# Optimization experiments

Measured on AMD Instinct MI355X. Metric: run time of the kernel, lower is better.

## Reference

```python
import jax, jax.numpy as jnp
import numpy as np

D_MODEL = 2048
N_HEAD = 16
N_KV_HEAD = 4
D_HEAD = D_MODEL // N_HEAD  # 128
WINDOW = 512
B, T = 2, 2048


def _rope_tables(T, d_head, base=10000.0):
    inv = 1.0 / (base ** (np.arange(0, d_head, 2, dtype=np.float32) / d_head))
    t = np.arange(T, dtype=np.float32)
    freqs = np.outer(t, inv)  # [T, d_head//2]
    return jnp.asarray(np.cos(freqs)), jnp.asarray(np.sin(freqs))


def setup_inputs() -> dict:
    key = jax.random.key(0)
    ks = jax.random.split(key, 5)
    cos, sin = _rope_tables(T, D_HEAD)
    s = 1.0 / np.sqrt(D_MODEL)
    return {
        "x": jax.random.normal(ks[0], (B, T, D_MODEL), jnp.float32),
        "cos": cos,
        "sin": sin,
        "Wq": jax.random.normal(ks[1], (D_MODEL, D_MODEL), jnp.float32) * s,
        "Wk": jax.random.normal(ks[2], (D_MODEL, N_KV_HEAD * D_HEAD), jnp.float32) * s,
        "Wv": jax.random.normal(ks[3], (D_MODEL, N_KV_HEAD * D_HEAD), jnp.float32) * s,
        "Wo": jax.random.normal(ks[4], (D_MODEL, D_MODEL), jnp.float32) * s,
    }


def _apply_rope(t, cos, sin):
    # t: [B, T, H, D]; cos/sin: [T, D//2]; interleaved-pair (complex) rotation
    tr = t[..., 0::2]
    ti = t[..., 1::2]
    c = cos[None, :, None, :]
    s = sin[None, :, None, :]
    out_r = tr * c - ti * s
    out_i = tr * s + ti * c
    return jnp.stack([out_r, out_i], axis=-1).reshape(t.shape)


def reference(x, cos, sin, Wq, Wk, Wv, Wo):
    Bx, Tx, C = x.shape
    q = (x @ Wq).reshape(Bx, Tx, N_HEAD, D_HEAD)       # [B,T,H,D]
    k = (x @ Wk).reshape(Bx, Tx, N_KV_HEAD, D_HEAD)    # [B,T,Hkv,D]
    v = (x @ Wv).reshape(Bx, Tx, N_KV_HEAD, D_HEAD)
    q = _apply_rope(q, cos, sin)
    k = _apply_rope(k, cos, sin)
    n_rep = N_HEAD // N_KV_HEAD
    k = jnp.repeat(k, n_rep, axis=2)  # [B,T,H,D]
    v = jnp.repeat(v, n_rep, axis=2)
    scale = 1.0 / np.sqrt(D_HEAD)
    att = jnp.einsum("bihd,bjhd->bhij", q, k) * scale  # [B,H,T,T]
    i = jnp.arange(Tx)[:, None]
    j = jnp.arange(Tx)[None, :]
    mask = (j <= i) & (j >= i - WINDOW + 1)            # causal sliding window
    att = jnp.where(mask[None, None], att, -jnp.inf)
    att = jax.nn.softmax(att, axis=-1)
    y = jnp.einsum("bhij,bjhd->bihd", att, v).reshape(Bx, Tx, C)
    return y @ Wo
```

## Files before the change

kernel.cpp:

```cpp
#include <hip/hip_runtime.h>
#include <hip/hip_bf16.h>
#include <cstdint>
#include <cstddef>

#define B_ 2
#define T_ 2048
#define NH 16
#define NKV 4
#define DH 128
#define DM 2048
#define WIN 512

typedef __attribute__((ext_vector_type(4))) float f32x4;
typedef __attribute__((ext_vector_type(8))) __bf16 bf16x8;

using bf16 = __hip_bfloat16;

__device__ inline void gload_lds16(const void* g, void* l) {
  __builtin_amdgcn_global_load_lds(
      (const __attribute__((address_space(1))) void*)g,
      (__attribute__((address_space(3))) void*)l, 16, 0, 0);
}

__device__ inline unsigned pack_bf2(float a, float b) {
  unsigned short ua = __builtin_bit_cast(unsigned short, __float2bfloat16(a));
  unsigned short ub = __builtin_bit_cast(unsigned short, __float2bfloat16(b));
  return (unsigned)ua | ((unsigned)ub << 16);
}

#define FBAR()                           \
  do {                                   \
    asm volatile("" ::: "memory");       \
    __builtin_amdgcn_s_barrier();        \
    asm volatile("" ::: "memory");       \
  } while (0)

__global__ void k_f32_to_bf16(const float* __restrict__ in, bf16* __restrict__ out, int n) {
  int i = (blockIdx.x * blockDim.x + threadIdx.x) * 4;
  if (i >= n) return;
  float4 v = *(const float4*)(in + i);
  ushort4 o;
  o.x = __builtin_bit_cast(unsigned short, __float2bfloat16(v.x));
  o.y = __builtin_bit_cast(unsigned short, __float2bfloat16(v.y));
  o.z = __builtin_bit_cast(unsigned short, __float2bfloat16(v.z));
  o.w = __builtin_bit_cast(unsigned short, __float2bfloat16(v.w));
  *(ushort4*)(out + i) = o;
}

__global__ __launch_bounds__(256) void k_transpose_bf16(const float* __restrict__ W,
                                                        bf16* __restrict__ Wt, int K, int N) {
  __shared__ float tile[64][65];
  int n0 = blockIdx.x * 64, k0 = blockIdx.y * 64;
  int tx = threadIdx.x & 63, tg = threadIdx.x >> 6;
#pragma unroll
  for (int r = 0; r < 16; ++r) {
    int k = tg * 16 + r;
    tile[k][tx] = W[(size_t)(k0 + k) * N + n0 + tx];
  }
  __syncthreads();
#pragma unroll
  for (int r = 0; r < 16; ++r) {
    int nn = tg * 16 + r;
    Wt[(size_t)(n0 + nn) * K + k0 + tx] = __float2bfloat16(tile[tx][nn]);
  }
}

template <int BN, bool OUT_BF16>
__global__ __launch_bounds__(512, 2) void k_gemm8(const bf16* __restrict__ A,
                                                  const bf16* __restrict__ Bt,
                                                  void* __restrict__ Cout,
                                                  int M, int N, int K) {
  constexpr int NR = BN / 64;
  constexpr int NHF = NR / 2;
  constexpr int BISS = BN / 128;
  __shared__ __align__(16) char As_[2][32768];
  __shared__ __align__(16) char Bs_[2][BN * 128];

  const int tid = threadIdx.x;
  const int w = tid >> 6, lane = tid & 63;
  const int li = lane & 15, g = lane >> 4;
  const int wm = w >> 2, wn = w & 3;

  const int nwg = gridDim.x * gridDim.y;
  int bid = blockIdx.y * gridDim.x + blockIdx.x;
  bid = (bid & 7) * (nwg >> 3) + (bid >> 3);
  const int m0 = (bid / gridDim.x) * 256;
  const int n0 = (bid % gridDim.x) * BN;

  const int ntiles = K >> 6;
  const int NT2 = ntiles >> 1;

  auto sA = [&](int buf, int tile, int half, int issue) {
    if (tile >= ntiles) return;
    const int R0 = half * 64 + issue * 128;
    const int rr = R0 + w * 8 + (lane >> 3);
    const int sl = lane & 7;
    const bf16* src = A + (size_t)(m0 + rr) * K + tile * 64 + ((sl ^ (rr & 7)) * 8);
    gload_lds16(src, As_[buf] + (R0 + w * 8) * 128);
  };
  auto sB = [&](int buf, int tile, int half, int issue) {
    if (tile >= ntiles) return;
    const int bb = issue * 8 + w;
    const int block = (BN == 256) ? ((bb >> 2) * 8 + (bb & 3) + half * 4)
                                  : ((bb >> 1) * 4 + (bb & 1) + half * 2);
    const int rr = block * 8 + (lane >> 3);
    const int sl = lane & 7;
    const bf16* src = Bt + (size_t)(n0 + rr) * K + tile * 64 + ((sl ^ (rr & 7)) * 8);
    gload_lds16(src, Bs_[buf] + block * 1024);
  };

  const int swz0 = (g ^ (li & 7)) * 16;
  const int swz1 = ((4 + g) ^ (li & 7)) * 16;
  bf16x8 af[8], b0v[NHF * 2], b1v[NHF * 2];
  f32x4 acc[8][NR] = {};

  auto readA = [&](int buf, int mh) {
#pragma unroll
    for (int m = 0; m < 4; ++m) {
      const char* p = As_[buf] + (wm * 128 + mh * 64 + m * 16 + li) * 128;
      af[m * 2 + 0] = *(const bf16x8*)(p + swz0);
      af[m * 2 + 1] = *(const bf16x8*)(p + swz1);
    }
  };
  auto readB = [&](int buf, int nh, bf16x8* bv) {
#pragma unroll
    for (int n = 0; n < NHF; ++n) {
      const char* p = Bs_[buf] + (wn * (NR * 16) + nh * (NHF * 16) + n * 16 + li) * 128;
      bv[n * 2 + 0] = *(const bf16x8*)(p + swz0);
      bv[n * 2 + 1] = *(const bf16x8*)(p + swz1);
    }
  };
  auto MMA = [&](int mh, int nh, const bf16x8* bv) {
    __builtin_amdgcn_s_setprio(1);
#pragma unroll
    for (int m = 0; m < 4; ++m)
#pragma unroll
      for (int n = 0; n < NHF; ++n)
#pragma unroll
        for (int kk = 0; kk < 2; ++kk)
          acc[mh * 4 + m][nh * NHF + n] = __builtin_amdgcn_mfma_f32_16x16x32_bf16(
              af[m * 2 + kk], bv[n * 2 + kk], acc[mh * 4 + m][nh * NHF + n], 0, 0, 0);
    __builtin_amdgcn_s_setprio(0);
  };
  auto VMW = [&](bool last) {
    if (last) {
      asm volatile("s_waitcnt vmcnt(0)" ::: "memory");
    } else {
      if constexpr (BN == 256)
        asm volatile("s_waitcnt vmcnt(4)" ::: "memory");
      else
        asm volatile("s_waitcnt vmcnt(3)" ::: "memory");
    }
    __builtin_amdgcn_sched_barrier(0);
  };

  sA(0, 0, 0, 0); sA(0, 0, 0, 1); sA(0, 0, 1, 0); sA(0, 0, 1, 1);
  sB(0, 0, 0, 0); if constexpr (BISS == 2) sB(0, 0, 0, 1);
  sB(0, 0, 1, 0); if constexpr (BISS == 2) sB(0, 0, 1, 1);
  sA(1, 1, 0, 0); sA(1, 1, 0, 1);
  sB(1, 1, 0, 0); if constexpr (BISS == 2) sB(1, 1, 0, 1);
  if constexpr (BN == 256)
    asm volatile("s_waitcnt vmcnt(4)" ::: "memory");
  else
    asm volatile("s_waitcnt vmcnt(3)" ::: "memory");
  __builtin_amdgcn_sched_barrier(0);
  FBAR();

  for (int itr = 0; itr < NT2; ++itr) {
    const int t = itr * 2;
    const bool last = (itr == NT2 - 1);
    readA(0, 0); readB(0, 0, b0v);
    sA(1, t + 1, 1, 0); sA(1, t + 1, 1, 1);
    FBAR(); MMA(0, 0, b0v); FBAR();
    readB(0, 1, b1v);
    sB(1, t + 1, 1, 0); if constexpr (BISS == 2) sB(1, t + 1, 1, 1);
    FBAR(); MMA(0, 1, b1v); FBAR();
    readA(0, 1);
    sA(0, t + 2, 0, 0); sA(0, t + 2, 0, 1);
    FBAR(); MMA(1, 0, b0v); FBAR();
    sB(0, t + 2, 0, 0); if constexpr (BISS == 2) sB(0, t + 2, 0, 1);
    VMW(last);
    FBAR(); MMA(1, 1, b1v); FBAR();
    readA(1, 0); readB(1, 0, b0v);
    sA(0, t + 2, 1, 0); sA(0, t + 2, 1, 1);
    FBAR(); MMA(0, 0, b0v); FBAR();
    readB(1, 1, b1v);
    sB(0, t + 2, 1, 0); if constexpr (BISS == 2) sB(0, t + 2, 1, 1);
    FBAR(); MMA(0, 1, b1v); FBAR();
    readA(1, 1);
    sA(1, t + 3, 0, 0); sA(1, t + 3, 0, 1);
    FBAR(); MMA(1, 0, b0v); FBAR();
    sB(1, t + 3, 0, 0); if constexpr (BISS == 2) sB(1, t + 3, 0, 1);
    VMW(last);
    FBAR(); MMA(1, 1, b1v); FBAR();
  }

#pragma unroll
  for (int mf = 0; mf < 8; ++mf)
#pragma unroll
    for (int nf = 0; nf < NR; ++nf)
#pragma unroll
      for (int r = 0; r < 4; ++r) {
        int row = m0 + wm * 128 + mf * 16 + g * 4 + r;
        int col = n0 + wn * (NR * 16) + nf * 16 + li;
        float v = acc[mf][nf][r];
        if constexpr (OUT_BF16)
          ((bf16*)Cout)[(size_t)row * N + col] = __float2bfloat16(v);
        else
          ((float*)Cout)[(size_t)row * N + col] = v;
      }
}

__global__ void k_rope_qkv(bf16* __restrict__ qkv, const float* __restrict__ cosT,
                           const float* __restrict__ sinT) {
  int p = blockIdx.x * blockDim.x + threadIdx.x;
  int i = p & 63;
  int h20 = (p >> 6) % 20;
  int bt = p / (64 * 20);
  int t = bt & (T_ - 1);
  float c = cosT[t * 64 + i], s = sinT[t * 64 + i];
  bool isq = h20 < 16;
  int col = isq ? h20 * DH : DM + (h20 - 16) * DH;
  float sc = isq ? 0.08838834764831845f : 1.0f;
  size_t base = (size_t)bt * 3072 + col + 2 * i;
  float tr = __bfloat162float(qkv[base]);
  float ti = __bfloat162float(qkv[base + 1]);
  qkv[base] = __float2bfloat16((tr * c - ti * s) * sc);
  qkv[base + 1] = __float2bfloat16((tr * s + ti * c) * sc);
}

__global__ __launch_bounds__(256) void k_vtrans(const bf16* __restrict__ qkv,
                                                bf16* __restrict__ vt) {
  __shared__ bf16 tile[64][72];
  int bt0 = blockIdx.x * 64, c0 = blockIdx.y * 64;
  int tx = threadIdx.x & 63, tg = threadIdx.x >> 6;
#pragma unroll
  for (int r = 0; r < 16; ++r) {
    int row = tg * 16 + r;
    tile[row][tx] = qkv[(size_t)(bt0 + row) * 3072 + 2560 + c0 + tx];
  }
  __syncthreads();
#pragma unroll
  for (int r = 0; r < 16; ++r) {
    int row2 = tg * 16 + r;
    vt[(size_t)(c0 + row2) * (B_ * T_) + bt0 + tx] = tile[tx][row2];
  }
}

__global__ __launch_bounds__(512) void k_attn(const bf16* __restrict__ qkv,
                                              const bf16* __restrict__ vt,
                                              bf16* __restrict__ Y) {
  __shared__ __align__(16) char Ks[2][9216];
  __shared__ __align__(16) char Vs[2][10240];
  __shared__ __align__(16) char Pl[8][1280];
  const int lane = threadIdx.x & 63;
  const int w = threadIdx.x >> 6;
  const int li = lane & 15, g = lane >> 4;
  const int t0 = ((int)gridDim.x - 1 - (int)blockIdx.x) * 32;
  const int b = blockIdx.y / NKV, kvh = blockIdx.y % NKV;
  const int h = kvh * 4 + (w >> 1);
  const int qrow0 = t0 + (w & 1) * 16;
  const int t = qrow0 + li;

  bf16x8 qf[4];
  const bf16* qbase = qkv + (size_t)(b * T_ + qrow0 + li) * 3072 + h * DH;
#pragma unroll
  for (int dk = 0; dk < 4; ++dk) qf[dk] = *(const bf16x8*)(qbase + dk * 32 + g * 8);

  float mrow = -1e4f;
  float srow = 0.f;
  f32x4 acc[8] = {};

  int ks0 = t0 - (WIN - 1);
  if (ks0 < 0) ks0 = 0;
  ks0 &= ~31;
  const int nt = (t0 + 31 - ks0) / 32 + 1;

  const bf16* kgbase = qkv + (size_t)(b * T_) * 3072 + DM + kvh * DH;
  const bf16* vgbase = vt + (size_t)(kvh * DH) * (B_ * T_) + b * T_;

  auto STAGE = [&](int buf, int kt) {
    for (int c = w; c < 19; c += 8) {
      if (c < 9) {
        int slot = c * 64 + lane;
        int row = slot / 17, cc = slot % 17;
        if (slot >= 544) { row = 0; cc = 0; }
        if (cc == 16) cc = 0;
        const bf16* src = kgbase + (size_t)(kt + row) * 3072 + cc * 8;
        gload_lds16(src, Ks[buf] + c * 1024);
      } else {
        int c2 = c - 9;
        int slot = c2 * 64 + lane;
        int row = slot / 5, cc = slot % 5;
        if (cc == 4) cc = 0;
        const bf16* src = vgbase + (size_t)row * (B_ * T_) + kt + cc * 8;
        gload_lds16(src, Vs[buf] + c2 * 1024);
      }
    }
  };

  STAGE(0, ks0);
  __syncthreads();
  int cur = 0;

  for (int it = 0; it < nt; ++it) {
    const int kt = ks0 + it * 32;
    if (it + 1 < nt) STAGE(cur ^ 1, kt + 32);

    f32x4 sc[2] = {};
#pragma unroll
    for (int n = 0; n < 2; ++n)
#pragma unroll
      for (int dk = 0; dk < 4; ++dk) {
        bf16x8 kf = *(const bf16x8*)(Ks[cur] + (n * 16 + li) * 272 + dk * 64 + g * 16);
        sc[n] = __builtin_amdgcn_mfma_f32_16x16x32_bf16(kf, qf[dk], sc[n], 0, 0, 0);
      }

    float p[2][4];
    float pmax = -1e30f;
#pragma unroll
    for (int n = 0; n < 2; ++n)
#pragma unroll
      for (int r = 0; r < 4; ++r) {
        int key = kt + n * 16 + g * 4 + r;
        bool valid = (key <= t) && (key > t - WIN);
        float pv = valid ? sc[n][r] : -1e30f;
        p[n][r] = pv;
        pmax = fmaxf(pmax, pv);
      }
    pmax = fmaxf(pmax, __shfl_xor(pmax, 16));
    pmax = fmaxf(pmax, __shfl_xor(pmax, 32));

    float nm = fmaxf(mrow, pmax);
    float alpha = __expf(mrow - nm);
    mrow = nm;
    float rs = 0.f;
#pragma unroll
    for (int n = 0; n < 2; ++n)
#pragma unroll
      for (int r = 0; r < 4; ++r) {
        p[n][r] = __expf(p[n][r] - nm);
        rs += p[n][r];
      }
    rs += __shfl_xor(rs, 16);
    rs += __shfl_xor(rs, 32);
    srow = srow * alpha + rs;

#pragma unroll
    for (int n = 0; n < 2; ++n) {
      *(unsigned*)(Pl[w] + li * 80 + n * 32 + g * 8) = pack_bf2(p[n][0], p[n][1]);
      *(unsigned*)(Pl[w] + li * 80 + n * 32 + g * 8 + 4) = pack_bf2(p[n][2], p[n][3]);
    }

    float af_[4];
#pragma unroll
    for (int r = 0; r < 4; ++r) af_[r] = __shfl(alpha, (g << 2) + r);
#pragma unroll
    for (int db = 0; db < 8; ++db)
#pragma unroll
      for (int r = 0; r < 4; ++r) acc[db][r] *= af_[r];

    bf16x8 pf = *(const bf16x8*)(Pl[w] + li * 80 + g * 16);
#pragma unroll
    for (int db = 0; db < 8; ++db) {
      bf16x8 vf = *(const bf16x8*)(Vs[cur] + (db * 16 + li) * 80 + g * 16);
      acc[db] = __builtin_amdgcn_mfma_f32_16x16x32_bf16(pf, vf, acc[db], 0, 0, 0);
    }

    __syncthreads();
    cur ^= 1;
  }

  float inv[4];
#pragma unroll
  for (int r = 0; r < 4; ++r) inv[r] = 1.f / __shfl(srow, (g << 2) + r);
  bf16* ybase = Y + (size_t)(b * T_ + qrow0 + (g << 2)) * DM + h * DH;
#pragma unroll
  for (int r = 0; r < 4; ++r)
#pragma unroll
    for (int db = 0; db < 8; ++db)
      ybase[(size_t)r * DM + db * 16 + li] = __float2bfloat16(acc[db][r] * inv[r]);
}

extern "C" void kernel_launch(void* const* d_in, const int* in_sizes, int n_in,
                              void* d_out, int out_size, void* d_ws, size_t ws_size,
                              hipStream_t stream) {
  const float* x = (const float*)d_in[0];
  const float* cosT = (const float*)d_in[1];
  const float* sinT = (const float*)d_in[2];
  const float* Wq = (const float*)d_in[3];
  const float* Wk = (const float*)d_in[4];
  const float* Wv = (const float*)d_in[5];
  const float* Wo = (const float*)d_in[6];
  float* out = (float*)d_out;

  char* ws = (char*)d_ws;
  bf16* xb = (bf16*)ws;     ws += (size_t)4096 * 2048 * 2;
  bf16* Wqkvt = (bf16*)ws;  ws += (size_t)3072 * 2048 * 2;
  bf16* Wot = (bf16*)ws;    ws += (size_t)2048 * 2048 * 2;
  bf16* qkv = (bf16*)ws;    ws += (size_t)4096 * 3072 * 2;
  bf16* yb = xb;
  bf16* vt = Wqkvt;

  k_f32_to_bf16<<<(4096 * 2048 / 4 + 255) / 256, 256, 0, stream>>>(x, xb, 4096 * 2048);
  k_transpose_bf16<<<dim3(2048 / 64, 2048 / 64), 256, 0, stream>>>(Wq, Wqkvt, 2048, 2048);
  k_transpose_bf16<<<dim3(512 / 64, 2048 / 64), 256, 0, stream>>>(Wk, Wqkvt + (size_t)2048 * 2048, 2048, 512);
  k_transpose_bf16<<<dim3(512 / 64, 2048 / 64), 256, 0, stream>>>(Wv, Wqkvt + (size_t)2560 * 2048, 2048, 512);
  k_transpose_bf16<<<dim3(2048 / 64, 2048 / 64), 256, 0, stream>>>(Wo, Wot, 2048, 2048);

  k_gemm8<256, true><<<dim3(3072 / 256, 4096 / 256), 512, 0, stream>>>(xb, Wqkvt, qkv, 4096, 3072, 2048);

  k_rope_qkv<<<(4096 * 20 * 64) / 256, 256, 0, stream>>>(qkv, cosT, sinT);
  k_vtrans<<<dim3(4096 / 64, 512 / 64), 256, 0, stream>>>(qkv, vt);

  k_attn<<<dim3(T_ / 32, B_ * NKV), 512, 0, stream>>>(qkv, vt, yb);

  k_gemm8<128, false><<<dim3(2048 / 128, 4096 / 256), 512, 0, stream>>>(yb, Wot, out, 4096, 2048, 2048);
}
```

Before: 183.6 us.

## Fuse prep and rope/vtrans launches and use 192-wide QKV GEMM tile

Merges the x conversion and four weight transposes into one kernel, and rope with the V transpose into another, cutting launch overhead. Generalizes the GEMM B-tile loader to support an uneven split, so the QKV GEMM can use a 192-wide tile giving 256 workgroups to better fill the GPU. Risk: uneven wave work and a different vmcnt accounting in the pipeline.

```diff
diff --git a/kernel.cpp b/kernel.cpp
--- a/kernel.cpp
+++ b/kernel.cpp
@@ -35,23 +35,41 @@
     asm volatile("" ::: "memory");       \
   } while (0)
 
-__global__ void k_f32_to_bf16(const float* __restrict__ in, bf16* __restrict__ out, int n) {
-  int i = (blockIdx.x * blockDim.x + threadIdx.x) * 4;
-  if (i >= n) return;
-  float4 v = *(const float4*)(in + i);
-  ushort4 o;
-  o.x = __builtin_bit_cast(unsigned short, __float2bfloat16(v.x));
-  o.y = __builtin_bit_cast(unsigned short, __float2bfloat16(v.y));
-  o.z = __builtin_bit_cast(unsigned short, __float2bfloat16(v.z));
-  o.w = __builtin_bit_cast(unsigned short, __float2bfloat16(v.w));
-  *(ushort4*)(out + i) = o;
-}
-
-__global__ __launch_bounds__(256) void k_transpose_bf16(const float* __restrict__ W,
-                                                        bf16* __restrict__ Wt, int K, int N) {
+__global__ __launch_bounds__(256) void k_prep(const float* __restrict__ x,
+                                              const float* __restrict__ Wq,
+                                              const float* __restrict__ Wk,
+                                              const float* __restrict__ Wv,
+                                              const float* __restrict__ Wo,
+                                              bf16* __restrict__ xb,
+                                              bf16* __restrict__ Wqkvt,
+                                              bf16* __restrict__ Wot) {
+  int id = blockIdx.x;
+  int tid = threadIdx.x;
+  if (id >= 2560) {
+    size_t base = (size_t)(id - 2560) * 4096 + tid * 16;
+#pragma unroll
+    for (int j = 0; j < 4; ++j) {
+      float4 v = *(const float4*)(x + base + j * 4);
+      ushort4 o;
+      o.x = __builtin_bit_cast(unsigned short, __float2bfloat16(v.x));
+      o.y = __builtin_bit_cast(unsigned short, __float2bfloat16(v.y));
+      o.z = __builtin_bit_cast(unsigned short, __float2bfloat16(v.z));
+      o.w = __builtin_bit_cast(unsigned short, __float2bfloat16(v.w));
+      *(ushort4*)(xb + base + j * 4) = o;
+    }
+    return;
+  }
+  const float* W;
+  bf16* Wt;
+  int N, bx, by;
+  if (id < 1024) { W = Wq; Wt = Wqkvt; N = 2048; bx = id & 31; by = id >> 5; }
+  else if (id < 1280) { id -= 1024; W = Wk; Wt = Wqkvt + (size_t)2048 * 2048; N = 512; bx = id & 7; by = id >> 3; }
+  else if (id < 1536) { id -= 1280; W = Wv; Wt = Wqkvt + (size_t)2560 * 2048; N = 512; bx = id & 7; by = id >> 3; }
+  else { id -= 1536; W = Wo; Wt = Wot; N = 2048; bx = id & 31; by = id >> 5; }
+
   __shared__ float tile[64][65];
-  int n0 = blockIdx.x * 64, k0 = blockIdx.y * 64;
-  int tx = threadIdx.x & 63, tg = threadIdx.x >> 6;
+  int n0 = bx * 64, k0 = by * 64;
+  int tx = tid & 63, tg = tid >> 6;
 #pragma unroll
   for (int r = 0; r < 16; ++r) {
     int k = tg * 16 + r;
@@ -61,7 +79,7 @@
 #pragma unroll
   for (int r = 0; r < 16; ++r) {
     int nn = tg * 16 + r;
-    Wt[(size_t)(n0 + nn) * K + k0 + tx] = __float2bfloat16(tile[tx][nn]);
+    Wt[(size_t)(n0 + nn) * 2048 + k0 + tx] = __float2bfloat16(tile[tx][nn]);
   }
 }
 
@@ -71,8 +89,9 @@
                                                   void* __restrict__ Cout,
                                                   int M, int N, int K) {
   constexpr int NR = BN / 64;
-  constexpr int NHF = NR / 2;
-  constexpr int BISS = BN / 128;
+  constexpr int NH0 = (NR + 1) / 2;
+  constexpr int NH1 = NR - NH0;
+  constexpr int VMN = 2 + NH0;
   __shared__ __align__(16) char As_[2][32768];
   __shared__ __align__(16) char Bs_[2][BN * 128];
 
@@ -100,18 +119,23 @@
   };
   auto sB = [&](int buf, int tile, int half, int issue) {
     if (tile >= ntiles) return;
-    const int bb = issue * 8 + w;
-    const int block = (BN == 256) ? ((bb >> 2) * 8 + (bb & 3) + half * 4)
-                                  : ((bb >> 1) * 4 + (bb & 1) + half * 2);
+    const int slot = issue * 8 + w;
+    const int per = (half ? NH1 : NH0) * 2;
+    const int wng = slot / per, within = slot % per;
+    const int block = wng * (NR * 2) + (half ? NH0 * 2 : 0) + within;
     const int rr = block * 8 + (lane >> 3);
     const int sl = lane & 7;
     const bf16* src = Bt + (size_t)(n0 + rr) * K + tile * 64 + ((sl ^ (rr & 7)) * 8);
     gload_lds16(src, Bs_[buf] + block * 1024);
   };
+  auto sBh = [&](int buf, int tile, int half) {
+    sB(buf, tile, half, 0);
+    if ((half ? NH1 : NH0) == 2) sB(buf, tile, half, 1);
+  };
 
   const int swz0 = (g ^ (li & 7)) * 16;
   const int swz1 = ((4 + g) ^ (li & 7)) * 16;
-  bf16x8 af[8], b0v[NHF * 2], b1v[NHF * 2];
+  bf16x8 af[8], b0v[NH0 * 2], b1v[NH1 * 2];
   f32x4 acc[8][NR] = {};
 
   auto readA = [&](int buf, int mh) {
@@ -122,31 +146,51 @@
       af[m * 2 + 1] = *(const bf16x8*)(p + swz1);
     }
   };
-  auto readB = [&](int buf, int nh, bf16x8* bv) {
-#pragma unroll
-    for (int n = 0; n < NHF; ++n) {
-      const char* p = Bs_[buf] + (wn * (NR * 16) + nh * (NHF * 16) + n * 16 + li) * 128;
-      bv[n * 2 + 0] = *(const bf16x8*)(p + swz0);
-      bv[n * 2 + 1] = *(const bf16x8*)(p + swz1);
-    }
-  };
-  auto MMA = [&](int mh, int nh, const bf16x8* bv) {
+  auto readB0 = [&](int buf) {
+#pragma unroll
+    for (int n = 0; n < NH0; ++n) {
+      const char* p = Bs_[buf] + (wn * (NR * 16) + n * 16 + li) * 128;
+      b0v[n * 2 + 0] = *(const bf16x8*)(p + swz0);
+      b0v[n * 2 + 1] = *(const bf16x8*)(p + swz1);
+    }
+  };
+  auto readB1 = [&](int buf) {
+#pragma unroll
+    for (int n = 0; n < NH1; ++n) {
+      const char* p = Bs_[buf] + (wn * (NR * 16) + NH0 * 16 + n * 16 + li) * 128;
+      b1v[n * 2 + 0] = *(const bf16x8*)(p + swz0);
+      b1v[n * 2 + 1] = *(const bf16x8*)(p + swz1);
+    }
+  };
+  auto MMA0 = [&](int mh) {
     __builtin_amdgcn_s_setprio(1);
 #pragma unroll
     for (int m = 0; m < 4; ++m)
 #pragma unroll
-      for (int n = 0; n < NHF; ++n)
+      for (int n = 0; n < NH0; ++n)
 #pragma unroll
         for (int kk = 0; kk < 2; ++kk)
-          acc[mh * 4 + m][nh * NHF + n] = __builtin_amdgcn_mfma_f32_16x16x32_bf16(
-              af[m * 2 + kk], bv[n * 2 + kk], acc[mh * 4 + m][nh * NHF + n], 0, 0, 0);
+          acc[mh * 4 + m][n] = __builtin_amdgcn_mfma_f32_16x16x32_bf16(
+              af[m * 2 + kk], b0v[n * 2 + kk], acc[mh * 4 + m][n], 0, 0, 0);
+    __builtin_amdgcn_s_setprio(0);
+  };
+  auto MMA1 = [&](int mh) {
+    __builtin_amdgcn_s_setprio(1);
+#pragma unroll
+    for (int m = 0; m < 4; ++m)
+#pragma unroll
+      for (int n = 0; n < NH1; ++n)
+#pragma unroll
+        for (int kk = 0; kk < 2; ++kk)
+          acc[mh * 4 + m][NH0 + n] = __builtin_amdgcn_mfma_f32_16x16x32_bf16(
+              af[m * 2 + kk], b1v[n * 2 + kk], acc[mh * 4 + m][NH0 + n], 0, 0, 0);
     __builtin_amdgcn_s_setprio(0);
   };
   auto VMW = [&](bool last) {
     if (last) {
       asm volatile("s_waitcnt vmcnt(0)" ::: "memory");
     } else {
-      if constexpr (BN == 256)
+      if constexpr (VMN == 4)
         asm volatile("s_waitcnt vmcnt(4)" ::: "memory");
       else
         asm volatile("s_waitcnt vmcnt(3)" ::: "memory");
@@ -155,11 +199,10 @@
   };
 
   sA(0, 0, 0, 0); sA(0, 0, 0, 1); sA(0, 0, 1, 0); sA(0, 0, 1, 1);
-  sB(0, 0, 0, 0); if constexpr (BISS == 2) sB(0, 0, 0, 1);
-  sB(0, 0, 1, 0); if constexpr (BISS == 2) sB(0, 0, 1, 1);
+  sBh(0, 0, 0); sBh(0, 0, 1);
   sA(1, 1, 0, 0); sA(1, 1, 0, 1);
-  sB(1, 1, 0, 0); if constexpr (BISS == 2) sB(1, 1, 0, 1);
-  if constexpr (BN == 256)
+  sBh(1, 1, 0);
+  if constexpr (VMN == 4)
     asm volatile("s_waitcnt vmcnt(4)" ::: "memory");
   else
     asm volatile("s_waitcnt vmcnt(3)" ::: "memory");
@@ -169,30 +212,30 @@
   for (int itr = 0; itr < NT2; ++itr) {
     const int t = itr * 2;
     const bool last = (itr == NT2 - 1);
-    readA(0, 0); readB(0, 0, b0v);
+    readA(0, 0); readB0(0);
     sA(1, t + 1, 1, 0); sA(1, t + 1, 1, 1);
-    FBAR(); MMA(0, 0, b0v); FBAR();
-    readB(0, 1, b1v);
-    sB(1, t + 1, 1, 0); if constexpr (BISS == 2) sB(1, t + 1, 1, 1);
-    FBAR(); MMA(0, 1, b1v); FBAR();
+    FBAR(); MMA0(0); FBAR();
+    readB1(0);
+    sBh(1, t + 1, 1);
+    FBAR(); MMA1(0); FBAR();
     readA(0, 1);
     sA(0, t + 2, 0, 0); sA(0, t + 2, 0, 1);
-    FBAR(); MMA(1, 0, b0v); FBAR();
-    sB(0, t + 2, 0, 0); if constexpr (BISS == 2) sB(0, t + 2, 0, 1);
+    FBAR(); MMA0(1); FBAR();
+    sBh(0, t + 2, 0);
     VMW(last);
-    FBAR(); MMA(1, 1, b1v); FBAR();
-    readA(1, 0); readB(1, 0, b0v);
+    FBAR(); MMA1(1); FBAR();
+    readA(1, 0); readB0(1);
     sA(0, t + 2, 1, 0); sA(0, t + 2, 1, 1);
-    FBAR(); MMA(0, 0, b0v); FBAR();
-    readB(1, 1, b1v);
-    sB(0, t + 2, 1, 0); if constexpr (BISS == 2) sB(0, t + 2, 1, 1);
-    FBAR(); MMA(0, 1, b1v); FBAR();
+    FBAR(); MMA0(0); FBAR();
+    readB1(1);
+    sBh(0, t + 2, 1);
+    FBAR(); MMA1(0); FBAR();
     readA(1, 1);
     sA(1, t + 3, 0, 0); sA(1, t + 3, 0, 1);
-    FBAR(); MMA(1, 0, b0v); FBAR();
-    sB(1, t + 3, 0, 0); if constexpr (BISS == 2) sB(1, t + 3, 0, 1);
+    FBAR(); MMA0(1); FBAR();
+    sBh(1, t + 3, 0);
     VMW(last);
-    FBAR(); MMA(1, 1, b1v); FBAR();
+    FBAR(); MMA1(1); FBAR();
   }
 
 #pragma unroll
@@ -211,29 +254,33 @@
       }
 }
 
-__global__ void k_rope_qkv(bf16* __restrict__ qkv, const float* __restrict__ cosT,
-                           const float* __restrict__ sinT) {
-  int p = blockIdx.x * blockDim.x + threadIdx.x;
-  int i = p & 63;
-  int h20 = (p >> 6) % 20;
-  int bt = p / (64 * 20);
-  int t = bt & (T_ - 1);
-  float c = cosT[t * 64 + i], s = sinT[t * 64 + i];
-  bool isq = h20 < 16;
-  int col = isq ? h20 * DH : DM + (h20 - 16) * DH;
-  float sc = isq ? 0.08838834764831845f : 1.0f;
-  size_t base = (size_t)bt * 3072 + col + 2 * i;
-  float tr = __bfloat162float(qkv[base]);
-  float ti = __bfloat162float(qkv[base + 1]);
-  qkv[base] = __float2bfloat16((tr * c - ti * s) * sc);
-  qkv[base + 1] = __float2bfloat16((tr * s + ti * c) * sc);
-}
-
-__global__ __launch_bounds__(256) void k_vtrans(const bf16* __restrict__ qkv,
-                                                bf16* __restrict__ vt) {
+__global__ __launch_bounds__(256) void k_rope_vtrans(bf16* __restrict__ qkv,
+                                                     const float* __restrict__ cosT,
+                                                     const float* __restrict__ sinT,
+                                                     bf16* __restrict__ vt) {
+  int id = blockIdx.x;
+  int tid = threadIdx.x;
+  if (id < 20480) {
+    int p = id * 256 + tid;
+    int i = p & 63;
+    int h20 = (p >> 6) % 20;
+    int bt = p / (64 * 20);
+    int t = bt & (T_ - 1);
+    float c = cosT[t * 64 + i], s = sinT[t * 64 + i];
+    bool isq = h20 < 16;
+    int col = isq ? h20 * DH : DM + (h20 - 16) * DH;
+    float sc = isq ? 0.08838834764831845f : 1.0f;
+    size_t base = (size_t)bt * 3072 + col + 2 * i;
+    float tr = __bfloat162float(qkv[base]);
+    float ti = __bfloat162float(qkv[base + 1]);
+    qkv[base] = __float2bfloat16((tr * c - ti * s) * sc);
+    qkv[base + 1] = __float2bfloat16((tr * s + ti * c) * sc);
+    return;
+  }
+  int v = id - 20480;
   __shared__ bf16 tile[64][72];
-  int bt0 = blockIdx.x * 64, c0 = blockIdx.y * 64;
-  int tx = threadIdx.x & 63, tg = threadIdx.x >> 6;
+  int bt0 = (v & 63) * 64, c0 = (v >> 6) * 64;
+  int tx = tid & 63, tg = tid >> 6;
 #pragma unroll
   for (int r = 0; r < 16; ++r) {
     int row = tg * 16 + r;
@@ -402,16 +449,11 @@
   bf16* yb = xb;
   bf16* vt = Wqkvt;
 
-  k_f32_to_bf16<<<(4096 * 2048 / 4 + 255) / 256, 256, 0, stream>>>(x, xb, 4096 * 2048);
-  k_transpose_bf16<<<dim3(2048 / 64, 2048 / 64), 256, 0, stream>>>(Wq, Wqkvt, 2048, 2048);
-  k_transpose_bf16<<<dim3(512 / 64, 2048 / 64), 256, 0, stream>>>(Wk, Wqkvt + (size_t)2048 * 2048, 2048, 512);
-  k_transpose_bf16<<<dim3(512 / 64, 2048 / 64), 256, 0, stream>>>(Wv, Wqkvt + (size_t)2560 * 2048, 2048, 512);
-  k_transpose_bf16<<<dim3(2048 / 64, 2048 / 64), 256, 0, stream>>>(Wo, Wot, 2048, 2048);
-
-  k_gemm8<256, true><<<dim3(3072 / 256, 4096 / 256), 512, 0, stream>>>(xb, Wqkvt, qkv, 4096, 3072, 2048);
-
-  k_rope_qkv<<<(4096 * 20 * 64) / 256, 256, 0, stream>>>(qkv, cosT, sinT);
-  k_vtrans<<<dim3(4096 / 64, 512 / 64), 256, 0, stream>>>(qkv, vt);
+  k_prep<<<4608, 256, 0, stream>>>(x, Wq, Wk, Wv, Wo, xb, Wqkvt, Wot);
+
+  k_gemm8<192, true><<<dim3(3072 / 192, 4096 / 256), 512, 0, stream>>>(xb, Wqkvt, qkv, 4096, 3072, 2048);
+
+  k_rope_vtrans<<<20992, 256, 0, stream>>>(qkv, cosT, sinT, vt);
 
   k_attn<<<dim3(T_ / 32, B_ * NKV), 512, 0, stream>>>(qkv, vt, yb);
 
```

Result: faster. 171.8 us (-6.5%).
